# Kernel optimization log

Measured on AMD Instinct MI355X. Metric: run time of the kernel, lower is better.

Reference implementation:

```python
import jax, jax.numpy as jnp
import numpy as np

HIDDEN = 768
NUM_LABELS = 25


def setup_inputs() -> dict:
    key = jax.random.key(0)
    k1, k2, k3, k4, k5 = jax.random.split(key, 5)
    B, H, S, E = 2, 12, 256, 64
    attention_probs = jax.random.uniform(k1, (B, H, S, S), dtype=jnp.float32)
    value_attentions = jax.random.normal(k2, (B, H, S, E), dtype=jnp.float32)
    relative_positions = jax.random.normal(k3, (B, S, S, H * E), dtype=jnp.float32)
    # nn.Linear(hidden_size, num_labels): weight [L, hidden], bias [L]
    bound = 1.0 / np.sqrt(HIDDEN)
    W = jax.random.uniform(k4, (NUM_LABELS, HIDDEN), dtype=jnp.float32, minval=-bound, maxval=bound)
    b = jax.random.uniform(k5, (NUM_LABELS,), dtype=jnp.float32, minval=-bound, maxval=bound)
    return {
        "attention_probs": attention_probs,
        "value_attentions": value_attentions,
        "relative_positions": relative_positions,
        "W": W,
        "b": b,
    }


def reference(attention_probs, value_attentions, relative_positions, W, b):
    B, H, S, E = value_attentions.shape
    # out[b,h,i,j,e] = probs[b,h,i,j] * (value[b,h,j,e] + rel[b,h,i,j,e])
    p = attention_probs[..., None]                      # [B,H,S,S,1]
    v = value_attentions[:, :, None, :, :]              # [B,H,1,S,E] broadcast over i
    rel = relative_positions.reshape(B, S, S, H, E).transpose(0, 3, 1, 2, 4)  # [B,H,S,S,E]
    out = p * (v + rel)                                 # [B,H,i,j,E]
    # permute(0,3,2,1,4) -> [B, j, i, H, E] -> [B,S,S,H*E]
    out = out.transpose(0, 3, 2, 1, 4).reshape(B, S, S, H * E)
    out = out @ W.T + b                                 # [B,S,S,L]
    return out.transpose(0, 1, 3, 2)                    # [B,S,L,S]
```

## Files before the change

### kernel.cpp

```cpp
#include <hip/hip_runtime.h>

#define NB 2
#define NH 12
#define NS 256
#define NE 64
#define NC 768
#define NL 25

__global__ __launch_bounds__(320) void tmhs_main(
    const float* __restrict__ p,
    const float* __restrict__ v,
    const float* __restrict__ rel,
    const float* __restrict__ W,
    const float* __restrict__ bias,
    float* __restrict__ out)
{
    __shared__ float sR[64][68];
    __shared__ float sW[NL][64];
    __shared__ float sP[64];
    __shared__ float sBias[NL];

    const int tid = threadIdx.x;
    const int bx  = blockIdx.x;
    const int it  = bx & 3;
    const int j   = (bx >> 2) & 255;
    const int b   = bx >> 10;
    const int i0  = it * 64;

    if (tid < NL) sBias[tid] = bias[tid];

    const int i_local = tid & 63;
    const int wv = tid >> 6;
    const int l0 = wv * 5;

    float acc[5] = {0.f, 0.f, 0.f, 0.f, 0.f};

    for (int k = 0; k < NH; ++k) {
        __syncthreads();
        if (tid < 256) {
            const int row  = tid >> 2;
            const int part = tid & 3;
            const float4* vs = (const float4*)(v + (((b*NH + k)*NS + j) << 6) + part*16);
            const float4* rs = (const float4*)(rel + (((b*NS + (i0+row))*NS + j)*NC + k*64 + part*16));
            float4* dst = (float4*)(&sR[row][part*16]);
            float4 a0 = rs[0], a1 = rs[1], a2 = rs[2], a3 = rs[3];
            const float4 b0 = vs[0], b1 = vs[1], b2 = vs[2], b3 = vs[3];
            a0.x += b0.x; a0.y += b0.y; a0.z += b0.z; a0.w += b0.w;
            a1.x += b1.x; a1.y += b1.y; a1.z += b1.z; a1.w += b1.w;
            a2.x += b2.x; a2.y += b2.y; a2.z += b2.z; a2.w += b2.w;
            a3.x += b3.x; a3.y += b3.y; a3.z += b3.z; a3.w += b3.w;
            dst[0] = a0; dst[1] = a1; dst[2] = a2; dst[3] = a3;
        } else {
            const int t = tid - 256;
            sP[t] = p[((b*NH + k)*NS + (i0 + t))*NS + j];
            for (int q = t; q < NL*16; q += 64) {
                ((float4*)sW)[q] = *((const float4*)(W + (q >> 4)*NC + k*64 + ((q & 15) << 2)));
            }
        }
        __syncthreads();

        const float pk = sP[i_local];
        float racc[5] = {0.f, 0.f, 0.f, 0.f, 0.f};
        #pragma unroll
        for (int e4 = 0; e4 < 16; ++e4) {
            const float4 r4 = *((const float4*)(&sR[i_local][e4*4]));
            #pragma unroll
            for (int u = 0; u < 5; ++u) {
                const float4 w4 = *((const float4*)(&sW[l0 + u][e4*4]));
                racc[u] = fmaf(r4.x, w4.x, racc[u]);
                racc[u] = fmaf(r4.y, w4.y, racc[u]);
                racc[u] = fmaf(r4.z, w4.z, racc[u]);
                racc[u] = fmaf(r4.w, w4.w, racc[u]);
            }
        }
        #pragma unroll
        for (int u = 0; u < 5; ++u) acc[u] = fmaf(pk, racc[u], acc[u]);
    }

    const int obase = ((b*NS + j)*NL)*NS + i0 + i_local;
    #pragma unroll
    for (int u = 0; u < 5; ++u) {
        out[obase + (l0 + u)*NS] = acc[u] + sBias[l0 + u];
    }
}

extern "C" void kernel_launch(void* const* d_in, const int* in_sizes, int n_in,
                              void* d_out, int out_size, void* d_ws, size_t ws_size,
                              hipStream_t stream) {
    const float* p    = (const float*)d_in[0];
    const float* v    = (const float*)d_in[1];
    const float* rel  = (const float*)d_in[2];
    const float* W    = (const float*)d_in[3];
    const float* bias = (const float*)d_in[4];
    float* out = (float*)d_out;
    tmhs_main<<<dim3(NB * NS * 4), dim3(320), 0, stream>>>(p, v, rel, W, bias, out);
}
```

Before: 660.1 us.

## Process all 256 query rows per block with register tiling and half-head chunks

```diff
diff --git a/kernel.cpp b/kernel.cpp
--- a/kernel.cpp
+++ b/kernel.cpp
@@ -6,6 +6,9 @@
 #define NE 64
 #define NC 768
 #define NL 25
+#define EC 32
+#define NIT 24
+#define SRS 36
 
 __global__ __launch_bounds__(320) void tmhs_main(
     const float* __restrict__ p,
@@ -15,73 +18,85 @@
     const float* __restrict__ bias,
     float* __restrict__ out)
 {
-    __shared__ float sR[64][68];
-    __shared__ float sW[NL][64];
-    __shared__ float sP[64];
-    __shared__ float sBias[NL];
+    __shared__ float sR[NS][SRS];
+    __shared__ float sW[NL][EC];
+    __shared__ float sBias[32];
 
     const int tid = threadIdx.x;
-    const int bx  = blockIdx.x;
-    const int it  = bx & 3;
-    const int j   = (bx >> 2) & 255;
-    const int b   = bx >> 10;
-    const int i0  = it * 64;
+    const int j   = blockIdx.x & 255;
+    const int b   = blockIdx.x >> 8;
 
     if (tid < NL) sBias[tid] = bias[tid];
 
-    const int i_local = tid & 63;
-    const int wv = tid >> 6;
-    const int l0 = wv * 5;
+    const int ig = tid & 63;
+    const int lg = tid >> 6;
+    const int l0 = lg * 5;
 
-    float acc[5] = {0.f, 0.f, 0.f, 0.f, 0.f};
+    float acc[4][5];
+#pragma unroll
+    for (int q = 0; q < 4; ++q)
+#pragma unroll
+        for (int u = 0; u < 5; ++u) acc[q][u] = 0.f;
 
-    for (int k = 0; k < NH; ++k) {
+    const int rbase = tid >> 2;
+    const int part  = tid & 3;
+
+    for (int m = 0; m < NIT; ++m) {
+        const int k  = m >> 1;
+        const int eh = (m & 1) << 5;
         __syncthreads();
         if (tid < 256) {
-            const int row  = tid >> 2;
-            const int part = tid & 3;
-            const float4* vs = (const float4*)(v + (((b*NH + k)*NS + j) << 6) + part*16);
-            const float4* rs = (const float4*)(rel + (((b*NS + (i0+row))*NS + j)*NC + k*64 + part*16));
-            float4* dst = (float4*)(&sR[row][part*16]);
-            float4 a0 = rs[0], a1 = rs[1], a2 = rs[2], a3 = rs[3];
-            const float4 b0 = vs[0], b1 = vs[1], b2 = vs[2], b3 = vs[3];
-            a0.x += b0.x; a0.y += b0.y; a0.z += b0.z; a0.w += b0.w;
-            a1.x += b1.x; a1.y += b1.y; a1.z += b1.z; a1.w += b1.w;
-            a2.x += b2.x; a2.y += b2.y; a2.z += b2.z; a2.w += b2.w;
-            a3.x += b3.x; a3.y += b3.y; a3.z += b3.z; a3.w += b3.w;
-            dst[0] = a0; dst[1] = a1; dst[2] = a2; dst[3] = a3;
+            const float4* vp = (const float4*)(v + (((b*NH + k)*NS + j) << 6) + eh + part*8);
+            const float4 v0 = vp[0], v1 = vp[1];
+            const int pbase = ((b*NH + k)*NS)*NS + j;
+#pragma unroll
+            for (int q = 0; q < 4; ++q) {
+                const int r  = rbase + (q << 6);
+                const float pr = p[pbase + r*NS];
+                const float4* rs = (const float4*)(rel + ((b*NS + r)*NS + j)*NC + k*64 + eh + part*8);
+                float4 a0 = rs[0], a1 = rs[1];
+                a0.x = pr*(a0.x + v0.x); a0.y = pr*(a0.y + v0.y);
+                a0.z = pr*(a0.z + v0.z); a0.w = pr*(a0.w + v0.w);
+                a1.x = pr*(a1.x + v1.x); a1.y = pr*(a1.y + v1.y);
+                a1.z = pr*(a1.z + v1.z); a1.w = pr*(a1.w + v1.w);
+                float4* dst = (float4*)&sR[r][part*8];
+                dst[0] = a0; dst[1] = a1;
+            }
         } else {
             const int t = tid - 256;
-            sP[t] = p[((b*NH + k)*NS + (i0 + t))*NS + j];
-            for (int q = t; q < NL*16; q += 64) {
-                ((float4*)sW)[q] = *((const float4*)(W + (q >> 4)*NC + k*64 + ((q & 15) << 2)));
+            const int wcol = k*64 + eh;
+            for (int q2 = t; q2 < NL*8; q2 += 64) {
+                const int row = q2 >> 3, c4 = q2 & 7;
+                *(float4*)&sW[row][c4*4] = *(const float4*)(W + row*NC + wcol + c4*4);
             }
         }
         __syncthreads();
 
-        const float pk = sP[i_local];
-        float racc[5] = {0.f, 0.f, 0.f, 0.f, 0.f};
-        #pragma unroll
-        for (int e4 = 0; e4 < 16; ++e4) {
-            const float4 r4 = *((const float4*)(&sR[i_local][e4*4]));
-            #pragma unroll
-            for (int u = 0; u < 5; ++u) {
-                const float4 w4 = *((const float4*)(&sW[l0 + u][e4*4]));
-                racc[u] = fmaf(r4.x, w4.x, racc[u]);
-                racc[u] = fmaf(r4.y, w4.y, racc[u]);
-                racc[u] = fmaf(r4.z, w4.z, racc[u]);
-                racc[u] = fmaf(r4.w, w4.w, racc[u]);
-            }
+#pragma unroll
+        for (int e4 = 0; e4 < 8; ++e4) {
+            float4 r4[4], w4[5];
+#pragma unroll
+            for (int q = 0; q < 4; ++q) r4[q] = *(const float4*)&sR[ig + (q << 6)][e4*4];
+#pragma unroll
+            for (int u = 0; u < 5; ++u) w4[u] = *(const float4*)&sW[l0 + u][e4*4];
+#pragma unroll
+            for (int q = 0; q < 4; ++q)
+#pragma unroll
+                for (int u = 0; u < 5; ++u) {
+                    acc[q][u] = fmaf(r4[q].x, w4[u].x, acc[q][u]);
+                    acc[q][u] = fmaf(r4[q].y, w4[u].y, acc[q][u]);
+                    acc[q][u] = fmaf(r4[q].z, w4[u].z, acc[q][u]);
+                    acc[q][u] = fmaf(r4[q].w, w4[u].w, acc[q][u]);
+                }
         }
-        #pragma unroll
-        for (int u = 0; u < 5; ++u) acc[u] = fmaf(pk, racc[u], acc[u]);
     }
 
-    const int obase = ((b*NS + j)*NL)*NS + i0 + i_local;
-    #pragma unroll
-    for (int u = 0; u < 5; ++u) {
-        out[obase + (l0 + u)*NS] = acc[u] + sBias[l0 + u];
-    }
+    const int ob = ((b*NS + j)*NL)*NS;
+#pragma unroll
+    for (int u = 0; u < 5; ++u)
+#pragma unroll
+        for (int q = 0; q < 4; ++q)
+            out[ob + (l0 + u)*NS + ig + (q << 6)] = acc[q][u] + sBias[l0 + u];
 }
 
 extern "C" void kernel_launch(void* const* d_in, const int* in_sizes, int n_in,
@@ -93,5 +108,5 @@
     const float* W    = (const float*)d_in[3];
     const float* bias = (const float*)d_in[4];
     float* out = (float*)d_out;
-    tmhs_main<<<dim3(NB * NS * 4), dim3(320), 0, stream>>>(p, v, rel, W, bias, out);
+    tmhs_main<<<dim3(NB * NS), dim3(320), 0, stream>>>(p, v, rel, W, bias, out);
 }
```

Result: slower. 708.4 us (+7.3%).

## Read W via scalar loads, fold probs into staging, drop producer wave

Applied to the files above, without the earlier changes.

```diff
diff --git a/kernel.cpp b/kernel.cpp
--- a/kernel.cpp
+++ b/kernel.cpp
@@ -7,7 +7,7 @@
 #define NC 768
 #define NL 25
 
-__global__ __launch_bounds__(320) void tmhs_main(
+__global__ __launch_bounds__(256) void tmhs_main(
     const float* __restrict__ p,
     const float* __restrict__ v,
     const float* __restrict__ rel,
@@ -16,71 +16,61 @@
     float* __restrict__ out)
 {
     __shared__ float sR[64][68];
-    __shared__ float sW[NL][64];
-    __shared__ float sP[64];
-    __shared__ float sBias[NL];
 
     const int tid = threadIdx.x;
     const int bx  = blockIdx.x;
     const int it  = bx & 3;
     const int j   = (bx >> 2) & 255;
     const int b   = bx >> 10;
-    const int i0  = it * 64;
+    const int i0  = it << 6;
 
-    if (tid < NL) sBias[tid] = bias[tid];
+    const int ig = tid & 63;
+    const int wv = __builtin_amdgcn_readfirstlane(tid >> 6);
+    const int l0 = wv * 6;
 
-    const int i_local = tid & 63;
-    const int wv = tid >> 6;
-    const int l0 = wv * 5;
+    float acc[7] = {0.f,0.f,0.f,0.f,0.f,0.f,0.f};
 
-    float acc[5] = {0.f, 0.f, 0.f, 0.f, 0.f};
+    const int row  = tid >> 2;
+    const int part = tid & 3;
 
     for (int k = 0; k < NH; ++k) {
         __syncthreads();
-        if (tid < 256) {
-            const int row  = tid >> 2;
-            const int part = tid & 3;
-            const float4* vs = (const float4*)(v + (((b*NH + k)*NS + j) << 6) + part*16);
-            const float4* rs = (const float4*)(rel + (((b*NS + (i0+row))*NS + j)*NC + k*64 + part*16));
-            float4* dst = (float4*)(&sR[row][part*16]);
-            float4 a0 = rs[0], a1 = rs[1], a2 = rs[2], a3 = rs[3];
-            const float4 b0 = vs[0], b1 = vs[1], b2 = vs[2], b3 = vs[3];
-            a0.x += b0.x; a0.y += b0.y; a0.z += b0.z; a0.w += b0.w;
-            a1.x += b1.x; a1.y += b1.y; a1.z += b1.z; a1.w += b1.w;
-            a2.x += b2.x; a2.y += b2.y; a2.z += b2.z; a2.w += b2.w;
-            a3.x += b3.x; a3.y += b3.y; a3.z += b3.z; a3.w += b3.w;
-            dst[0] = a0; dst[1] = a1; dst[2] = a2; dst[3] = a3;
-        } else {
-            const int t = tid - 256;
-            sP[t] = p[((b*NH + k)*NS + (i0 + t))*NS + j];
-            for (int q = t; q < NL*16; q += 64) {
-                ((float4*)sW)[q] = *((const float4*)(W + (q >> 4)*NC + k*64 + ((q & 15) << 2)));
+        {
+            const float  pr = p[((b*NH + k)*NS + (i0 + row))*NS + j];
+            const float4* vp = (const float4*)(v + (((b*NH + k)*NS + j) << 6) + part*16);
+            const float4* rs = (const float4*)(rel + ((b*NS + (i0+row))*NS + j)*NC + k*64 + part*16);
+            float4* dst = (float4*)&sR[row][part*16];
+#pragma unroll
+            for (int q = 0; q < 4; ++q) {
+                float4 a = rs[q];
+                const float4 bb = vp[q];
+                a.x = pr*(a.x + bb.x); a.y = pr*(a.y + bb.y);
+                a.z = pr*(a.z + bb.z); a.w = pr*(a.w + bb.w);
+                dst[q] = a;
             }
         }
         __syncthreads();
 
-        const float pk = sP[i_local];
-        float racc[5] = {0.f, 0.f, 0.f, 0.f, 0.f};
-        #pragma unroll
+        const float* wk = W + k*64;
+#pragma unroll
         for (int e4 = 0; e4 < 16; ++e4) {
-            const float4 r4 = *((const float4*)(&sR[i_local][e4*4]));
-            #pragma unroll
-            for (int u = 0; u < 5; ++u) {
-                const float4 w4 = *((const float4*)(&sW[l0 + u][e4*4]));
-                racc[u] = fmaf(r4.x, w4.x, racc[u]);
-                racc[u] = fmaf(r4.y, w4.y, racc[u]);
-                racc[u] = fmaf(r4.z, w4.z, racc[u]);
-                racc[u] = fmaf(r4.w, w4.w, racc[u]);
+            const float4 r4 = *(const float4*)&sR[ig][e4*4];
+#pragma unroll
+            for (int u = 0; u < 7; ++u) {
+                const float4 w4 = *(const float4*)(wk + (l0 + u)*NC + e4*4);
+                acc[u] = fmaf(r4.x, w4.x, acc[u]);
+                acc[u] = fmaf(r4.y, w4.y, acc[u]);
+                acc[u] = fmaf(r4.z, w4.z, acc[u]);
+                acc[u] = fmaf(r4.w, w4.w, acc[u]);
             }
         }
-        #pragma unroll
-        for (int u = 0; u < 5; ++u) acc[u] = fmaf(pk, racc[u], acc[u]);
     }
 
-    const int obase = ((b*NS + j)*NL)*NS + i0 + i_local;
-    #pragma unroll
-    for (int u = 0; u < 5; ++u) {
-        out[obase + (l0 + u)*NS] = acc[u] + sBias[l0 + u];
+    const int ob = ((b*NS + j)*NL)*NS + i0 + ig;
+#pragma unroll
+    for (int u = 0; u < 7; ++u) {
+        const int l = l0 + u;
+        out[ob + l*NS] = acc[u] + bias[l];
     }
 }
 
@@ -93,5 +83,5 @@
     const float* W    = (const float*)d_in[3];
     const float* bias = (const float*)d_in[4];
     float* out = (float*)d_out;
-    tmhs_main<<<dim3(NB * NS * 4), dim3(320), 0, stream>>>(p, v, rel, W, bias, out);
+    tmhs_main<<<dim3(NB * NS * 4), dim3(256), 0, stream>>>(p, v, rel, W, bias, out);
 }
```

Measured after the change: 612.0 us. 1.08x faster.
